# Optimization experiments

Hardware: AMD Instinct MI355X
Metric: run time of the kernel (lower is better)

## Reference

```python
import jax, jax.numpy as jnp
import numpy as np
from jax import lax

H, W = 496, 432
NUM_CLASSES = 3
NUM_ROT = 2
A_PER_LOC = NUM_CLASSES * NUM_ROT  # 6
BOX = 7
NMS_PRE = 4096
MAX_NUM = 500
SCORE_THR = 0.1
NMS_THR = 0.5
PI = float(np.pi)


def _make_priors():
    # Anchor3DRangeGenerator equivalent: grid of BEV centers x (3 sizes x 2 rotations)
    xs = jnp.linspace(0.0, 69.12, W, dtype=jnp.float32)
    ys = jnp.linspace(-39.68, 39.68, H, dtype=jnp.float32)
    cy, cx = jnp.meshgrid(ys, xs, indexing='ij')  # [H,W]
    sizes = jnp.array([[3.9, 1.6, 1.56], [0.8, 0.6, 1.73], [1.76, 0.6, 1.73]], jnp.float32)
    szs = jnp.repeat(sizes, NUM_ROT, axis=0)                       # [6,3]
    rots = jnp.tile(jnp.array([0.0, 1.57], jnp.float32), NUM_CLASSES)  # [6]
    cx = jnp.broadcast_to(cx[:, :, None], (H, W, A_PER_LOC))
    cy = jnp.broadcast_to(cy[:, :, None], (H, W, A_PER_LOC))
    cz = jnp.full((H, W, A_PER_LOC), -1.78, jnp.float32)
    wlh = jnp.broadcast_to(szs[None, None], (H, W, A_PER_LOC, 3))
    r = jnp.broadcast_to(rots[None, None], (H, W, A_PER_LOC))
    pri = jnp.concatenate([cx[..., None], cy[..., None], cz[..., None], wlh, r[..., None]], -1)
    return pri.reshape(-1, BOX)  # [H*W*6, 7]


def setup_inputs() -> dict:
    key = jax.random.key(0)
    k1, k2, k3 = jax.random.split(key, 3)
    cls_score = jax.random.normal(k1, (A_PER_LOC * NUM_CLASSES, H, W), jnp.float32)
    bbox_pred = 0.1 * jax.random.normal(k2, (A_PER_LOC * BOX, H, W), jnp.float32)
    dir_cls_pred = jax.random.normal(k3, (A_PER_LOC * 2, H, W), jnp.float32)
    priors = _make_priors()
    return {"cls_score": cls_score, "bbox_pred": bbox_pred,
            "dir_cls_pred": dir_cls_pred, "priors": priors}


def _decode(anchors, deltas):
    xa, ya, za, wa, la, ha, ra = [anchors[:, i] for i in range(7)]
    xt, yt, zt, wt, lt, ht, rt = [deltas[:, i] for i in range(7)]
    za = za + ha / 2
    diag = jnp.sqrt(la ** 2 + wa ** 2)
    xg = xt * diag + xa
    yg = yt * diag + ya
    zg = zt * ha + za
    lg = jnp.exp(lt) * la
    wg = jnp.exp(wt) * wa
    hg = jnp.exp(ht) * ha
    rg = rt + ra
    zg = zg - hg / 2
    return jnp.stack([xg, yg, zg, wg, lg, hg, rg], axis=-1)


def _nms_keep(boxes_xyxy, scores_c, valid_c):
    # Greedy NMS with py_cpu_nms math (+1 pixel convention), fixed-shape masked version.
    n = boxes_xyxy.shape[0]
    order = jnp.argsort(-scores_c)
    b = boxes_xyxy[order]
    v = valid_c[order]
    x1, y1, x2, y2 = b[:, 0], b[:, 1], b[:, 2], b[:, 3]
    areas = (x2 - x1 + 1.0) * (y2 - y1 + 1.0)
    xx1 = jnp.maximum(x1[:, None], x1[None, :])
    yy1 = jnp.maximum(y1[:, None], y1[None, :])
    xx2 = jnp.minimum(x2[:, None], x2[None, :])
    yy2 = jnp.minimum(y2[:, None], y2[None, :])
    inter = jnp.maximum(0.0, xx2 - xx1 + 1.0) * jnp.maximum(0.0, yy2 - yy1 + 1.0)
    iou = inter / (areas[:, None] + areas[None, :] - inter)  # [N,N]
    idx = jnp.arange(n)

    def body(i, keep):
        row = (iou[i] > NMS_THR) & (idx > i)
        return jnp.where(keep[i], keep & ~row, keep)

    keep_sorted = lax.fori_loop(0, n, body, v)
    return jnp.zeros(n, bool).at[order].set(keep_sorted)


def reference(cls_score, bbox_pred, dir_cls_pred, priors):
    # flatten feature maps -> per-anchor predictions
    scores_all = jax.nn.sigmoid(cls_score.transpose(1, 2, 0).reshape(-1, NUM_CLASSES))  # [A,C]
    dir_all = jnp.argmax(dir_cls_pred.transpose(1, 2, 0).reshape(-1, 2), axis=-1)       # [A]
    bp_all = bbox_pred.transpose(1, 2, 0).reshape(-1, BOX)                               # [A,7]
    # nms_pre top-k by best class score
    max_scores = scores_all.max(axis=1)
    _, topk = lax.top_k(max_scores, NMS_PRE)
    pri = priors[topk]
    bp = bp_all[topk]
    sc = scores_all[topk]           # [N,C]
    dsc = dir_all[topk]             # [N]
    bboxes = _decode(pri, bp)       # [N,7] x,y,z,w,l,h,r
    # BEV box -> axis-aligned xyxy (stands in for open3d obb2aabb + xywhr2xyxyr)
    x, y, w, l = bboxes[:, 0], bboxes[:, 1], bboxes[:, 3], bboxes[:, 4]
    boxes_xyxy = jnp.stack([x - w / 2, y - l / 2, x + w / 2, y + l / 2], axis=-1)
    # per-class greedy NMS on the same candidate pool
    valid = sc > SCORE_THR          # [N,C]
    keep = jax.vmap(lambda s, v: _nms_keep(boxes_xyxy, s, v), in_axes=(1, 1))(sc, valid)  # [C,N]
    # merge classes, keep top max_num by score (fixed-shape, padded)
    comb = jnp.where(keep, sc.T, -jnp.inf)                # [C,N]
    top_scores, flat_idx = lax.top_k(comb.reshape(-1), MAX_NUM)
    labels = flat_idx // NMS_PRE
    bidx = flat_idx % NMS_PRE
    sel_b = bboxes[bidx]                                   # [MAX_NUM,7]
    sel_d = dsc[bidx].astype(sel_b.dtype)
    # direction-aware yaw fix (replicates original expression incl. precedence)
    r = sel_b[:, 6]
    dir_rot = r + PI / 2 - jnp.floor(r + 0.5) * PI
    sel_b = sel_b.at[:, 6].set(dir_rot - PI / 2 + PI * sel_d)
    valid_out = jnp.isfinite(top_scores)
    sel_b = jnp.where(valid_out[:, None], sel_b, 0.0)
    out_scores = jnp.where(valid_out, top_scores, 0.0)
    labels = jnp.where(valid_out, labels, -1)
    return sel_b, out_scores, labels
```

## Files before the change

kernel.cpp:

```cpp
#include <hip/hip_runtime.h>
#include <stdint.h>
#include <stddef.h>

constexpr int kH = 496, kW = 432;
constexpr int HWSZ = kH * kW;
constexpr int NANCH = HWSZ * 6;
constexpr int NPRE = 4096;
constexpr int MAXNUM = 500;
constexpr int CAND_CAP = 8192;
constexpr float SCORE_THR_F = 0.1f;
constexpr float PIF  = 3.14159265358979323846f;
constexpr float HPIF = 1.57079632679489661923f;

constexpr int NBINS  = 32768;
constexpr int NPAIR  = NBINS / 2;
constexpr int NB_H   = 256;
constexpr uint64_t PADKEY = 0xFFFFFFFF00000000ull;

constexpr size_t HIST_OFF  = 0;
constexpr size_t MISC_OFF  = 131072;
constexpr size_t VW_OFF    = 131328;
constexpr size_t ZERO_BYTES= 131328 + 1536;
constexpr size_t MS_OFF    = ZERO_BYTES;
constexpr size_t CAND_OFF  = MS_OFF + 4ull * NANCH;
constexpr size_t SC3_OFF   = CAND_OFF + 8ull * CAND_CAP;
constexpr size_t DSC_OFF   = SC3_OFF + 4ull * NPRE * 3;
constexpr size_t BB7_OFF   = DSC_OFF + 4ull * NPRE;
constexpr size_t BOX4_OFF  = BB7_OFF + 4ull * NPRE * 7;
constexpr size_t AREA_OFF  = BOX4_OFF + 4ull * NPRE * 4;
constexpr size_t ORD_OFF   = AREA_OFF + 4ull * NPRE;
constexpr size_t PMASK_OFF = ORD_OFF + 4ull * 3 * NPRE;
constexpr size_t KEEPW_OFF = PMASK_OFF + 8ull * 3 * NPRE * 64;
constexpr size_t OUTK_OFF  = KEEPW_OFF + 8ull * 3 * 64;
constexpr size_t DIAG_OFF  = OUTK_OFF + 8ull * 2048;

__device__ __forceinline__ float sigmoidf_(float x) { return 1.0f / (1.0f + expf(-x)); }

__device__ __forceinline__ uint64_t readlane64(uint64_t v, int lane) {
  uint32_t lo = (uint32_t)__builtin_amdgcn_readlane((int)(uint32_t)(v & 0xffffffffull), lane);
  uint32_t hi = (uint32_t)__builtin_amdgcn_readlane((int)(uint32_t)(v >> 32), lane);
  return (((uint64_t)hi) << 32) | (uint64_t)lo;
}

__device__ __forceinline__ void gl_lds16(const uint64_t* g, void* l) {
  __builtin_amdgcn_global_load_lds(
      (const __attribute__((address_space(1))) void*)g,
      (__attribute__((address_space(3))) void*)l, 16, 0, 0);
}
__device__ __forceinline__ void gl_lds4(const uint32_t* g, void* l) {
  __builtin_amdgcn_global_load_lds(
      (const __attribute__((address_space(1))) void*)g,
      (__attribute__((address_space(3))) void*)l, 4, 0, 0);
}


__global__ __launch_bounds__(256) void k_score(const float* __restrict__ cls,
                                               float* __restrict__ ms,
                                               uint32_t* __restrict__ hist) {
  __shared__ uint32_t h[NPAIR];
  const int t = threadIdx.x, blk = blockIdx.x;
  for (int i = t; i < NPAIR; i += 256) h[i] = 0;
  __syncthreads();
  for (int p = blk * 256 + t; p < HWSZ; p += NB_H * 256) {
#pragma unroll
    for (int k = 0; k < 6; ++k) {
      float s0 = sigmoidf_(cls[(k * 3 + 0) * HWSZ + p]);
      float s1 = sigmoidf_(cls[(k * 3 + 1) * HWSZ + p]);
      float s2 = sigmoidf_(cls[(k * 3 + 2) * HWSZ + p]);
      float m = fmaxf(s0, fmaxf(s1, s2));
      ms[p * 6 + k] = m;
      uint32_t bin = __float_as_uint(m) >> 15;
      atomicAdd(&h[bin >> 1], 1u << ((bin & 1) * 16));
    }
  }
  __syncthreads();
  for (int i = t; i < NPAIR; i += 256) {
    uint32_t v = h[i];
    if (v) {
      uint32_t lo = v & 0xFFFFu, hi = v >> 16;
      if (lo) atomicAdd(&hist[2 * i],     lo);
      if (hi) atomicAdd(&hist[2 * i + 1], hi);
    }
  }
}

__global__ __launch_bounds__(256) void k_compact(const float* __restrict__ ms,
                                                 const uint32_t* __restrict__ hist,
                                                 uint32_t* __restrict__ misc,
                                                 uint64_t* __restrict__ cand) {
  constexpr int APB = 4096;
  __shared__ uint64_t lbuf[APB];
  __shared__ uint32_t suf[256];
  __shared__ uint32_t win[256];
  __shared__ uint32_t lcnt, lbase, sWin, sAbove, sB;
  const int t = threadIdx.x;
  const int base = blockIdx.x * APB;

  uint32_t s = 0;
  const int hbase = t * 128;
#pragma unroll 16
  for (int i = 0; i < 128; ++i) s += hist[hbase + i];
  suf[t] = s;
  if (t == 0) { lcnt = 0; sB = 0; }
  __syncthreads();
  for (int d = 1; d < 256; d <<= 1) {
    uint32_t v = suf[t] + ((t + d < 256) ? suf[t + d] : 0u);
    __syncthreads(); suf[t] = v; __syncthreads();
  }
  {
    uint32_t sin = suf[t];
    uint32_t sup = (t < 255) ? suf[t + 1] : 0u;
    if (sin >= (uint32_t)NPRE && sup < (uint32_t)NPRE) { sWin = (uint32_t)t; sAbove = sup; }
  }
  __syncthreads();
  const uint32_t wbase = sWin * 128u;
  win[t] = (t < 128) ? hist[wbase + (uint32_t)t] : 0u;
  __syncthreads();
  for (int d = 1; d < 256; d <<= 1) {
    uint32_t v = win[t] + ((t + d < 256) ? win[t + d] : 0u);
    __syncthreads(); win[t] = v; __syncthreads();
  }
  if (t < 128 && sAbove + win[t] >= (uint32_t)NPRE)
    atomicMax(&sB, wbase + (uint32_t)t);
  __syncthreads();
  const uint32_t B = sB;

#pragma unroll
  for (int q = 0; q < 16; ++q) {
    int a = base + q * 256 + t;
    if (a < NANCH) {
      uint32_t bits = __float_as_uint(ms[a]);
      if ((bits >> 15) >= B) {
        uint32_t sl = atomicAdd(&lcnt, 1u);
        lbuf[sl] = (((uint64_t)(~bits)) << 32) | (uint32_t)a;
      }
    }
  }
  __syncthreads();
  const uint32_t n = lcnt;
  if (t == 0 && n > 0) lbase = atomicAdd(&misc[0], n);
  __syncthreads();
  if (n > 0) {
    const uint32_t b0 = lbase;
    for (uint32_t i = t; i < n; i += 256) {
      uint32_t slot = b0 + i;
      if (slot < (uint32_t)CAND_CAP) cand[slot] = lbuf[i];
    }
  }
}

__global__ __launch_bounds__(256) void k_rankgather(const uint64_t* __restrict__ cand,
                                                    const uint32_t* __restrict__ misc,
                                                    const float* __restrict__ cls,
                                                    const float* __restrict__ bbp,
                                                    const float* __restrict__ dirp,
                                                    const float* __restrict__ priors,
                                                    float* __restrict__ sc3,
                                                    uint32_t* __restrict__ dsc,
                                                    float* __restrict__ bb7,
                                                    float* __restrict__ box4,
                                                    float* __restrict__ areaA) {
  const int tid = threadIdx.x, ln = tid & 63;
  const int wave = blockIdx.x * 4 + (tid >> 6);
  const int base = wave * 8;
  uint32_t cnt = misc[0];
  if (cnt > (uint32_t)CAND_CAP) cnt = CAND_CAP;
  uint64_t kr[8];
#pragma unroll
  for (int r = 0; r < 8; ++r) kr[r] = cand[base + r];
  uint32_t rnk[8];
#pragma unroll
  for (int r = 0; r < 8; ++r) rnk[r] = 0;
  const int nch = ((int)cnt + 63) >> 6;
  for (int ch = 0; ch < nch; ++ch) {
    uint64_t ck = cand[ch * 64 + ln];
    uint64_t vm = __ballot(ch * 64 + ln < (int)cnt);
#pragma unroll
    for (int r = 0; r < 8; ++r)
      rnk[r] += (uint32_t)__popcll(__ballot(ck < kr[r]) & vm);
  }
  uint32_t my_a = 0, my_i = 0; int my_ok = 0;
#pragma unroll
  for (int r = 0; r < 8; ++r) {
    int ok = (base + r < (int)cnt) && (rnk[r] < (uint32_t)NPRE);
    if (ln == r) { my_a = (uint32_t)kr[r]; my_i = rnk[r]; my_ok = ok; }
  }
  if (ln < 8 && my_ok) {
    uint32_t a = my_a, i = my_i;
    uint32_t p = a / 6u;
    uint32_t k = a - p * 6u;
#pragma unroll
    for (int c = 0; c < 3; ++c) sc3[i * 3 + c] = sigmoidf_(cls[(k * 3 + c) * HWSZ + p]);
    float d0 = dirp[(k * 2 + 0) * HWSZ + p];
    float d1 = dirp[(k * 2 + 1) * HWSZ + p];
    dsc[i] = (d1 > d0) ? 1u : 0u;
    float dt[7], pr[7];
#pragma unroll
    for (int q = 0; q < 7; ++q) dt[q] = bbp[(k * 7 + q) * HWSZ + p];
#pragma unroll
    for (int q = 0; q < 7; ++q) pr[q] = priors[(size_t)a * 7 + q];
    float za = pr[2] + pr[5] * 0.5f;
    float diag = sqrtf(pr[4] * pr[4] + pr[3] * pr[3]);
    float xg = dt[0] * diag + pr[0];
    float yg = dt[1] * diag + pr[1];
    float zg = dt[2] * pr[5] + za;
    float wg = expf(dt[3]) * pr[3];
    float lg = expf(dt[4]) * pr[4];
    float hg = expf(dt[5]) * pr[5];
    float rg = dt[6] + pr[6];
    zg = zg - hg * 0.5f;
    bb7[i * 7 + 0] = xg; bb7[i * 7 + 1] = yg; bb7[i * 7 + 2] = zg;
    bb7[i * 7 + 3] = wg; bb7[i * 7 + 4] = lg; bb7[i * 7 + 5] = hg; bb7[i * 7 + 6] = rg;
    float x1 = xg - wg * 0.5f, y1 = yg - lg * 0.5f;
    float x2 = xg + wg * 0.5f, y2 = yg + lg * 0.5f;
    box4[i * 4 + 0] = x1; box4[i * 4 + 1] = y1; box4[i * 4 + 2] = x2; box4[i * 4 + 3] = y2;
    areaA[i] = (x2 - x1 + 1.0f) * (y2 - y1 + 1.0f);
  }
}

__global__ __launch_bounds__(256) void k_rankcls(const float* __restrict__ sc3,
                                                 uint32_t* __restrict__ ord,
                                                 unsigned long long* __restrict__ vw) {
  const int tid = threadIdx.x, ln = tid & 63;
  const int c = blockIdx.y;
  const int wave = blockIdx.x * 4 + (tid >> 6);
  const int base = wave * 8;
  uint64_t kr[8];
#pragma unroll
  for (int r = 0; r < 8; ++r) {
    int j = base + r;
    kr[r] = (((uint64_t)(~__float_as_uint(sc3[j * 3 + c]))) << 32) | (uint32_t)j;
  }
  uint32_t rnk[8];
#pragma unroll
  for (int r = 0; r < 8; ++r) rnk[r] = 0;
  for (int ch = 0; ch < NPRE / 64; ++ch) {
    int j = ch * 64 + ln;
    uint64_t ck = (((uint64_t)(~__float_as_uint(sc3[j * 3 + c]))) << 32) | (uint32_t)j;
#pragma unroll
    for (int r = 0; r < 8; ++r)
      rnk[r] += (uint32_t)__popcll(__ballot(ck < kr[r]));
  }
  uint32_t my_rnk = 0; int my_v = 0;
#pragma unroll
  for (int r = 0; r < 8; ++r) {
    uint32_t sb = ~(uint32_t)(kr[r] >> 32);
    int v = __uint_as_float(sb) > SCORE_THR_F;
    if (ln == r) { my_rnk = rnk[r]; my_v = v; }
  }
  if (ln < 8) {
    ord[c * NPRE + my_rnk] = (uint32_t)(base + ln);
    if (my_v) atomicOr(&vw[c * 64 + (my_rnk >> 6)], 1ull << (my_rnk & 63));
  }
}

__global__ __launch_bounds__(64) void k_mask(const uint32_t* __restrict__ ord,
                                             const float* __restrict__ box4,
                                             const float* __restrict__ areaA,
                                             uint64_t* __restrict__ pmask,
                                             uint64_t* __restrict__ diagv) {
  const int t = threadIdx.x;
  int task = blockIdx.x;
  const int c = task / 2080;
  int rr = task - c * 2080;
  int it = 0;
  while (rr >= 64 - it) { rr -= 64 - it; ++it; }
  const int jt = it + rr;

  __shared__ float jx1[64], jy1[64], jx2[64], jy2[64], jar[64];
  int j = ord[c * NPRE + jt * 64 + t];
  jx1[t] = box4[j * 4 + 0]; jy1[t] = box4[j * 4 + 1];
  jx2[t] = box4[j * 4 + 2]; jy2[t] = box4[j * 4 + 3];
  jar[t] = areaA[j];
  __syncthreads();
  int I = it * 64 + t;
  int i = ord[c * NPRE + I];
  float x1 = box4[i * 4 + 0], y1 = box4[i * 4 + 1];
  float x2 = box4[i * 4 + 2], y2 = box4[i * 4 + 3];
  float ar = areaA[i];
  uint64_t bits = 0;
  for (int b = 0; b < 64; ++b) {
    float xx1 = fmaxf(x1, jx1[b]), yy1 = fmaxf(y1, jy1[b]);
    float xx2 = fminf(x2, jx2[b]), yy2 = fminf(y2, jy2[b]);
    float iw = fmaxf(0.0f, xx2 - xx1 + 1.0f);
    float ih = fmaxf(0.0f, yy2 - yy1 + 1.0f);
    float inter = iw * ih;
    float iou = inter / (ar + jar[b] - inter);
    bits |= ((uint64_t)(iou > 0.5f)) << b;
  }
  pmask[((size_t)(c * NPRE + I)) * 64 + (size_t)jt] = bits;
  if (jt == it) diagv[(size_t)c * NPRE + (size_t)I] = bits;
}

__global__ __launch_bounds__(64) void k_nms(const uint64_t* __restrict__ pmask,
                                            const uint64_t* __restrict__ diagv,
                                            const unsigned long long* __restrict__ vw,
                                            uint64_t* __restrict__ keepw) {
  __shared__ uint64_t lb[3 * 4096];
  __shared__ uint64_t dl[4096];
  __shared__ uint64_t avl[64];
  const int c = blockIdx.x;
  const int ln = threadIdx.x;
  const uint64_t* pm = pmask + (size_t)c * NPRE * 64;

  const uint32_t* vw32 = (const uint32_t*)(vw + (size_t)c * 64);
  gl_lds4(vw32 + ln, avl);
  gl_lds4(vw32 + 64 + ln, (uint8_t*)avl + 256);
  const uint64_t* gd = diagv + (size_t)c * NPRE;
#pragma unroll
  for (int i = 0; i < 32; ++i) gl_lds16(gd + i * 128 + ln * 2, dl + i * 128);
#pragma unroll
  for (int i = 0; i < 32; ++i) gl_lds16(pm + i * 128 + ln * 2, lb + i * 128);
#pragma unroll
  for (int i = 0; i < 32; ++i) gl_lds16(pm + 4096 + i * 128 + ln * 2, lb + 4096 + i * 128);
  asm volatile("s_waitcnt vmcnt(32)" ::: "memory");
  __builtin_amdgcn_sched_barrier(0);

  uint64_t avail = avl[ln];
  uint64_t mykeep = 0;
  int cnt = 0;
  for (int T = 0; T < 64; ++T) {
    uint64_t dgT = dl[T * 64 + ln];
    if (T > 0) {
      if (T < 63) { asm volatile("s_waitcnt vmcnt(32)" ::: "memory"); }
      else        { asm volatile("s_waitcnt vmcnt(0)"  ::: "memory"); }
      __builtin_amdgcn_sched_barrier(0);
    }
    if (T + 2 < 64) {
      uint64_t* dst = lb + (size_t)((T + 2) % 3) * 4096;
      const uint64_t* gb = pm + ((size_t)(T + 2) << 12);
#pragma unroll
      for (int i = 0; i < 32; ++i) gl_lds16(gb + i * 128 + ln * 2, dst + i * 128);
    }

    uint64_t awT = readlane64(avail, T);
    if (awT) {
      uint64_t kwT;
      uint64_t conf = dgT & awT & ~(1ull << ln);
      bool bad = ((awT >> ln) & 1ull) && (conf != 0ull);
      if (__ballot(bad) == 0ull) {
        kwT = awT;
      } else {
        uint64_t aw = awT;
        kwT = 0;
        while (aw) {
          int r = (int)__builtin_ctzll(aw);
          kwT |= (1ull << r);
          aw &= ~(1ull << r);
          aw &= ~readlane64(dgT, r);
        }
      }
      if (ln == T) mykeep = kwT;
      cnt += (int)__popcll(kwT);
      if (cnt >= MAXNUM) break;

      const uint64_t* tb = lb + (size_t)(T % 3) * 4096;
      uint64_t supp = 0;
#pragma unroll
      for (int r = 0; r < 64; ++r) {
        uint64_t msk = (uint64_t)0 - ((kwT >> r) & 1ull);
        supp |= tb[r * 64 + ln] & msk;
      }
      avail &= ~supp;
      if (__ballot(ln > T && avail != 0) == 0ull) break;
    }
  }
  asm volatile("s_waitcnt vmcnt(0)" ::: "memory");
  keepw[c * 64 + ln] = mykeep;
}

__global__ __launch_bounds__(1024) void k_collect(const uint64_t* __restrict__ keepw,
                                                  const uint32_t* __restrict__ ord,
                                                  const float* __restrict__ sc3,
                                                  uint64_t* __restrict__ outk,
                                                  uint32_t* __restrict__ misc) {
  const int c = blockIdx.x, t = threadIdx.x, w = t >> 6, ln = t & 63;
  if (c == 3) {
    int i = 3 * MAXNUM + t;
    if (i < 2048) outk[i] = PADKEY;
    return;
  }
  __shared__ uint32_t wsum[16];
  uint32_t bits4 = 0;
#pragma unroll
  for (int q = 0; q < 4; ++q) {
    int i = t * 4 + q;
    uint32_t b = (uint32_t)((keepw[c * 64 + (i >> 6)] >> (i & 63)) & 1ull);
    bits4 |= b << q;
  }
  uint32_t cnt = __popc(bits4);
  uint32_t incl = cnt;
#pragma unroll
  for (int d = 1; d < 64; d <<= 1) { uint32_t u = __shfl_up(incl, d, 64); if (ln >= d) incl += u; }
  if (ln == 63) wsum[w] = incl;
  __syncthreads();
  uint32_t wb = 0, total = 0;
#pragma unroll
  for (int i = 0; i < 16; ++i) { uint32_t v = wsum[i]; total += v; if (i < w) wb += v; }
  uint32_t r = wb + incl - cnt;
#pragma unroll
  for (int q = 0; q < 4; ++q) {
    if ((bits4 >> q) & 1u) {
      if (r < (uint32_t)MAXNUM) {
        uint32_t pos = ord[c * NPRE + t * 4 + q];
        uint32_t sb = __float_as_uint(sc3[pos * 3 + c]);
        outk[c * MAXNUM + r] = (((uint64_t)(~sb)) << 32) | (uint32_t)(c * NPRE + pos);
      }
      ++r;
    }
  }
  uint32_t Vc = total < (uint32_t)MAXNUM ? total : (uint32_t)MAXNUM;
  if (t == 0) misc[8 + c] = Vc;
  for (uint32_t s = Vc + t; s < (uint32_t)MAXNUM; s += 1024)
    outk[c * MAXNUM + s] = PADKEY;
}

__global__ __launch_bounds__(256) void k_emit(const uint64_t* __restrict__ outk,
                                              const uint32_t* __restrict__ misc,
                                              const float* __restrict__ bb7,
                                              const uint32_t* __restrict__ dsc,
                                              float* __restrict__ out) {
  const int tid = threadIdx.x, ln = tid & 63;
  const int wave = blockIdx.x * 4 + (tid >> 6);
  const int base = wave * 8;
  uint64_t kr[8];
#pragma unroll
  for (int r = 0; r < 8; ++r) kr[r] = outk[base + r];
  uint32_t rnk[8];
#pragma unroll
  for (int r = 0; r < 8; ++r) rnk[r] = 0;
  for (int ch = 0; ch < 2048 / 64; ++ch) {
    uint64_t ck = outk[ch * 64 + ln];
#pragma unroll
    for (int r = 0; r < 8; ++r)
      rnk[r] += (uint32_t)__popcll(__ballot(ck < kr[r]));
  }
  if (ln == 0) {
#pragma unroll
    for (int r = 0; r < 8; ++r) {
      uint64_t key = kr[r];
      uint32_t rk = rnk[r];
      if (key != PADKEY && rk < (uint32_t)MAXNUM) {
        uint32_t flat = (uint32_t)key;
        float score = __uint_as_float(~((uint32_t)(key >> 32)));
        int cc = (int)(flat >> 12);
        int pos = (int)(flat & 4095u);
        const float* b = bb7 + (size_t)pos * 7;
        float rr0 = b[6];
        float dir_rot = rr0 + HPIF - floorf(rr0 + 0.5f) * PIF;
        float rr = dir_rot - HPIF + PIF * (float)dsc[pos];
#pragma unroll
        for (int q = 0; q < 6; ++q) out[rk * 7 + q] = b[q];
        out[rk * 7 + 6] = rr;
        out[7 * MAXNUM + rk] = score;
        out[8 * MAXNUM + rk] = (float)cc;
      }
    }
  }
  if (blockIdx.x == 0) {
    uint32_t V = misc[8] + misc[9] + misc[10];
    for (uint32_t s = V + tid; s < (uint32_t)MAXNUM; s += 256) {
#pragma unroll
      for (int q = 0; q < 7; ++q) out[s * 7 + q] = 0.0f;
      out[7 * MAXNUM + s] = 0.0f;
      out[8 * MAXNUM + s] = -1.0f;
    }
  }
}

extern "C" void kernel_launch(void* const* d_in, const int* in_sizes, int n_in,
                              void* d_out, int out_size, void* d_ws, size_t ws_size,
                              hipStream_t stream) {
  (void)in_sizes; (void)n_in; (void)out_size; (void)ws_size;
  const float* cls    = (const float*)d_in[0];
  const float* bbp    = (const float*)d_in[1];
  const float* dirp   = (const float*)d_in[2];
  const float* priors = (const float*)d_in[3];
  char* ws = (char*)d_ws;

  uint32_t* hist   = (uint32_t*)(ws + HIST_OFF);
  uint32_t* misc   = (uint32_t*)(ws + MISC_OFF);
  unsigned long long* vw = (unsigned long long*)(ws + VW_OFF);
  float*    ms     = (float*)(ws + MS_OFF);
  uint64_t* cand   = (uint64_t*)(ws + CAND_OFF);
  float*    sc3    = (float*)(ws + SC3_OFF);
  uint32_t* dsc    = (uint32_t*)(ws + DSC_OFF);
  float*    bb7    = (float*)(ws + BB7_OFF);
  float*    box4   = (float*)(ws + BOX4_OFF);
  float*    areaA  = (float*)(ws + AREA_OFF);
  uint32_t* ord    = (uint32_t*)(ws + ORD_OFF);
  uint64_t* pmask  = (uint64_t*)(ws + PMASK_OFF);
  uint64_t* keepw  = (uint64_t*)(ws + KEEPW_OFF);
  uint64_t* outk   = (uint64_t*)(ws + OUTK_OFF);
  uint64_t* diagv  = (uint64_t*)(ws + DIAG_OFF);

  hipMemsetAsync(ws, 0, ZERO_BYTES, stream);
  k_score<<<NB_H, 256, 0, stream>>>(cls, ms, hist);
  k_compact<<<(NANCH + 4095) / 4096, 256, 0, stream>>>(ms, hist, misc, cand);
  k_rankgather<<<256, 256, 0, stream>>>(cand, misc, cls, bbp, dirp, priors,
                                        sc3, dsc, bb7, box4, areaA);
  k_rankcls<<<dim3(128, 3), 256, 0, stream>>>(sc3, ord, vw);
  k_mask<<<6240, 64, 0, stream>>>(ord, box4, areaA, pmask, diagv);
  k_nms<<<3, 64, 0, stream>>>(pmask, diagv, vw, keepw);
  k_collect<<<4, 1024, 0, stream>>>(keepw, ord, sc3, outk, misc);
  k_emit<<<64, 256, 0, stream>>>(outk, misc, bb7, dsc, (float*)d_out);
}
```

Measured before the change: 259.1 us.

## Fuse NMS, collect and emit into one kernel with last-block merge

Replaces the separate k_nms, k_collect and k_emit launches with a single kernel. Each per-class block runs the greedy NMS, compacts its kept indices with a wave prefix scan, and the last block to finish (found with an atomic counter) merges the three sorted class lists by binary-search ranking and writes the output. The valid-score bitmask is now built with a ballot inside k_mask instead of atomicOr in k_rankcls, and the zeroed workspace is smaller. This removes two launches and their global round-trips, at the cost of a serial merge tail in one block and an atomic-counter handoff between blocks.

```diff
diff --git a/kernel.cpp b/kernel.cpp
--- a/kernel.cpp
+++ b/kernel.cpp
@@ -15,13 +15,12 @@
 constexpr int NBINS  = 32768;
 constexpr int NPAIR  = NBINS / 2;
 constexpr int NB_H   = 256;
-constexpr uint64_t PADKEY = 0xFFFFFFFF00000000ull;
 
 constexpr size_t HIST_OFF  = 0;
 constexpr size_t MISC_OFF  = 131072;
-constexpr size_t VW_OFF    = 131328;
-constexpr size_t ZERO_BYTES= 131328 + 1536;
-constexpr size_t MS_OFF    = ZERO_BYTES;
+constexpr size_t ZERO_BYTES= 131072 + 256;
+constexpr size_t VW_OFF    = ZERO_BYTES;
+constexpr size_t MS_OFF    = VW_OFF + 8ull * 3 * 64;
 constexpr size_t CAND_OFF  = MS_OFF + 4ull * NANCH;
 constexpr size_t SC3_OFF   = CAND_OFF + 8ull * CAND_CAP;
 constexpr size_t DSC_OFF   = SC3_OFF + 4ull * NPRE * 3;
@@ -30,9 +29,8 @@
 constexpr size_t AREA_OFF  = BOX4_OFF + 4ull * NPRE * 4;
 constexpr size_t ORD_OFF   = AREA_OFF + 4ull * NPRE;
 constexpr size_t PMASK_OFF = ORD_OFF + 4ull * 3 * NPRE;
-constexpr size_t KEEPW_OFF = PMASK_OFF + 8ull * 3 * NPRE * 64;
-constexpr size_t OUTK_OFF  = KEEPW_OFF + 8ull * 3 * 64;
-constexpr size_t DIAG_OFF  = OUTK_OFF + 8ull * 2048;
+constexpr size_t OUTK_OFF  = PMASK_OFF + 8ull * 3 * NPRE * 64;
+constexpr size_t DIAG_OFF  = OUTK_OFF + 8ull * 3 * MAXNUM;
 
 __device__ __forceinline__ float sigmoidf_(float x) { return 1.0f / (1.0f + expf(-x)); }
 
@@ -51,6 +49,15 @@
   __builtin_amdgcn_global_load_lds(
       (const __attribute__((address_space(1))) void*)g,
       (__attribute__((address_space(3))) void*)l, 4, 0, 0);
+}
+
+__device__ __forceinline__ uint32_t lbnd(const uint64_t* a, uint32_t n, uint64_t key) {
+  uint32_t lo = 0, hi = n;
+  while (lo < hi) {
+    uint32_t mid = (lo + hi) >> 1;
+    if (a[mid] < key) lo = mid + 1; else hi = mid;
+  }
+  return lo;
 }
 
 
@@ -219,8 +226,7 @@
 }
 
 __global__ __launch_bounds__(256) void k_rankcls(const float* __restrict__ sc3,
-                                                 uint32_t* __restrict__ ord,
-                                                 unsigned long long* __restrict__ vw) {
+                                                 uint32_t* __restrict__ ord) {
   const int tid = threadIdx.x, ln = tid & 63;
   const int c = blockIdx.y;
   const int wave = blockIdx.x * 4 + (tid >> 6);
@@ -241,24 +247,20 @@
     for (int r = 0; r < 8; ++r)
       rnk[r] += (uint32_t)__popcll(__ballot(ck < kr[r]));
   }
-  uint32_t my_rnk = 0; int my_v = 0;
-#pragma unroll
-  for (int r = 0; r < 8; ++r) {
-    uint32_t sb = ~(uint32_t)(kr[r] >> 32);
-    int v = __uint_as_float(sb) > SCORE_THR_F;
-    if (ln == r) { my_rnk = rnk[r]; my_v = v; }
-  }
-  if (ln < 8) {
-    ord[c * NPRE + my_rnk] = (uint32_t)(base + ln);
-    if (my_v) atomicOr(&vw[c * 64 + (my_rnk >> 6)], 1ull << (my_rnk & 63));
-  }
+  uint32_t my_rnk = 0;
+#pragma unroll
+  for (int r = 0; r < 8; ++r)
+    if (ln == r) my_rnk = rnk[r];
+  if (ln < 8) ord[c * NPRE + my_rnk] = (uint32_t)(base + ln);
 }
 
 __global__ __launch_bounds__(64) void k_mask(const uint32_t* __restrict__ ord,
                                              const float* __restrict__ box4,
                                              const float* __restrict__ areaA,
+                                             const float* __restrict__ sc3,
                                              uint64_t* __restrict__ pmask,
-                                             uint64_t* __restrict__ diagv) {
+                                             uint64_t* __restrict__ diagv,
+                                             unsigned long long* __restrict__ vwords) {
   const int t = threadIdx.x;
   int task = blockIdx.x;
   const int c = task / 2080;
@@ -289,158 +291,140 @@
     bits |= ((uint64_t)(iou > 0.5f)) << b;
   }
   pmask[((size_t)(c * NPRE + I)) * 64 + (size_t)jt] = bits;
-  if (jt == it) diagv[(size_t)c * NPRE + (size_t)I] = bits;
-}
-
-__global__ __launch_bounds__(64) void k_nms(const uint64_t* __restrict__ pmask,
-                                            const uint64_t* __restrict__ diagv,
-                                            const unsigned long long* __restrict__ vw,
-                                            uint64_t* __restrict__ keepw) {
+  if (jt == it) {
+    diagv[(size_t)c * NPRE + (size_t)I] = bits;
+    unsigned long long vm = __ballot(sc3[i * 3 + c] > SCORE_THR_F);
+    if (t == 0) vwords[c * 64 + it] = vm;
+  }
+}
+
+__global__ __launch_bounds__(256) void k_nmsce(const uint64_t* __restrict__ pmask,
+                                               const uint64_t* __restrict__ diagv,
+                                               const unsigned long long* __restrict__ vw,
+                                               const uint32_t* __restrict__ ord,
+                                               const float* __restrict__ sc3,
+                                               const float* __restrict__ bb7,
+                                               const uint32_t* __restrict__ dsc,
+                                               uint64_t* __restrict__ outk,
+                                               uint32_t* __restrict__ misc,
+                                               float* __restrict__ out) {
   __shared__ uint64_t lb[3 * 4096];
   __shared__ uint64_t dl[4096];
   __shared__ uint64_t avl[64];
+  __shared__ uint32_t sflag;
+  __shared__ uint32_t sV[3];
   const int c = blockIdx.x;
-  const int ln = threadIdx.x;
-  const uint64_t* pm = pmask + (size_t)c * NPRE * 64;
-
-  const uint32_t* vw32 = (const uint32_t*)(vw + (size_t)c * 64);
-  gl_lds4(vw32 + ln, avl);
-  gl_lds4(vw32 + 64 + ln, (uint8_t*)avl + 256);
-  const uint64_t* gd = diagv + (size_t)c * NPRE;
-#pragma unroll
-  for (int i = 0; i < 32; ++i) gl_lds16(gd + i * 128 + ln * 2, dl + i * 128);
-#pragma unroll
-  for (int i = 0; i < 32; ++i) gl_lds16(pm + i * 128 + ln * 2, lb + i * 128);
-#pragma unroll
-  for (int i = 0; i < 32; ++i) gl_lds16(pm + 4096 + i * 128 + ln * 2, lb + 4096 + i * 128);
-  asm volatile("s_waitcnt vmcnt(32)" ::: "memory");
-  __builtin_amdgcn_sched_barrier(0);
-
-  uint64_t avail = avl[ln];
-  uint64_t mykeep = 0;
-  int cnt = 0;
-  for (int T = 0; T < 64; ++T) {
-    uint64_t dgT = dl[T * 64 + ln];
-    if (T > 0) {
-      if (T < 63) { asm volatile("s_waitcnt vmcnt(32)" ::: "memory"); }
-      else        { asm volatile("s_waitcnt vmcnt(0)"  ::: "memory"); }
-      __builtin_amdgcn_sched_barrier(0);
-    }
-    if (T + 2 < 64) {
-      uint64_t* dst = lb + (size_t)((T + 2) % 3) * 4096;
-      const uint64_t* gb = pm + ((size_t)(T + 2) << 12);
-#pragma unroll
-      for (int i = 0; i < 32; ++i) gl_lds16(gb + i * 128 + ln * 2, dst + i * 128);
-    }
-
-    uint64_t awT = readlane64(avail, T);
-    if (awT) {
-      uint64_t kwT;
-      uint64_t conf = dgT & awT & ~(1ull << ln);
-      bool bad = ((awT >> ln) & 1ull) && (conf != 0ull);
-      if (__ballot(bad) == 0ull) {
-        kwT = awT;
-      } else {
-        uint64_t aw = awT;
-        kwT = 0;
-        while (aw) {
-          int r = (int)__builtin_ctzll(aw);
-          kwT |= (1ull << r);
-          aw &= ~(1ull << r);
-          aw &= ~readlane64(dgT, r);
+  const int t = threadIdx.x, ln = t & 63, wv = t >> 6;
+
+  if (wv == 0) {
+    const uint64_t* pm = pmask + (size_t)c * NPRE * 64;
+    const uint32_t* vw32 = (const uint32_t*)(vw + (size_t)c * 64);
+    gl_lds4(vw32 + ln, avl);
+    gl_lds4(vw32 + 64 + ln, (uint8_t*)avl + 256);
+    const uint64_t* gd = diagv + (size_t)c * NPRE;
+#pragma unroll
+    for (int i = 0; i < 32; ++i) gl_lds16(gd + i * 128 + ln * 2, dl + i * 128);
+#pragma unroll
+    for (int i = 0; i < 32; ++i) gl_lds16(pm + i * 128 + ln * 2, lb + i * 128);
+#pragma unroll
+    for (int i = 0; i < 32; ++i) gl_lds16(pm + 4096 + i * 128 + ln * 2, lb + 4096 + i * 128);
+    asm volatile("s_waitcnt vmcnt(32)" ::: "memory");
+    __builtin_amdgcn_sched_barrier(0);
+
+    uint64_t avail = avl[ln];
+    uint64_t mykeep = 0;
+    int cnt = 0;
+    for (int T = 0; T < 64; ++T) {
+      uint64_t dgT = dl[T * 64 + ln];
+      if (T > 0) {
+        if (T < 63) { asm volatile("s_waitcnt vmcnt(32)" ::: "memory"); }
+        else        { asm volatile("s_waitcnt vmcnt(0)"  ::: "memory"); }
+        __builtin_amdgcn_sched_barrier(0);
+      }
+      if (T + 2 < 64) {
+        uint64_t* dst = lb + (size_t)((T + 2) % 3) * 4096;
+        const uint64_t* gb = pm + ((size_t)(T + 2) << 12);
+#pragma unroll
+        for (int i = 0; i < 32; ++i) gl_lds16(gb + i * 128 + ln * 2, dst + i * 128);
+      }
+      uint64_t awT = readlane64(avail, T);
+      if (awT) {
+        uint64_t kwT;
+        uint64_t conf = dgT & awT & ~(1ull << ln);
+        bool bad = ((awT >> ln) & 1ull) && (conf != 0ull);
+        if (__ballot(bad) == 0ull) {
+          kwT = awT;
+        } else {
+          uint64_t aw = awT; kwT = 0;
+          while (aw) {
+            int r = (int)__builtin_ctzll(aw);
+            kwT |= (1ull << r);
+            aw &= ~(1ull << r);
+            aw &= ~readlane64(dgT, r);
+          }
         }
-      }
-      if (ln == T) mykeep = kwT;
-      cnt += (int)__popcll(kwT);
-      if (cnt >= MAXNUM) break;
-
-      const uint64_t* tb = lb + (size_t)(T % 3) * 4096;
-      uint64_t supp = 0;
-#pragma unroll
-      for (int r = 0; r < 64; ++r) {
-        uint64_t msk = (uint64_t)0 - ((kwT >> r) & 1ull);
-        supp |= tb[r * 64 + ln] & msk;
-      }
-      avail &= ~supp;
-      if (__ballot(ln > T && avail != 0) == 0ull) break;
-    }
-  }
-  asm volatile("s_waitcnt vmcnt(0)" ::: "memory");
-  keepw[c * 64 + ln] = mykeep;
-}
-
-__global__ __launch_bounds__(1024) void k_collect(const uint64_t* __restrict__ keepw,
-                                                  const uint32_t* __restrict__ ord,
-                                                  const float* __restrict__ sc3,
-                                                  uint64_t* __restrict__ outk,
-                                                  uint32_t* __restrict__ misc) {
-  const int c = blockIdx.x, t = threadIdx.x, w = t >> 6, ln = t & 63;
-  if (c == 3) {
-    int i = 3 * MAXNUM + t;
-    if (i < 2048) outk[i] = PADKEY;
-    return;
-  }
-  __shared__ uint32_t wsum[16];
-  uint32_t bits4 = 0;
-#pragma unroll
-  for (int q = 0; q < 4; ++q) {
-    int i = t * 4 + q;
-    uint32_t b = (uint32_t)((keepw[c * 64 + (i >> 6)] >> (i & 63)) & 1ull);
-    bits4 |= b << q;
-  }
-  uint32_t cnt = __popc(bits4);
-  uint32_t incl = cnt;
-#pragma unroll
-  for (int d = 1; d < 64; d <<= 1) { uint32_t u = __shfl_up(incl, d, 64); if (ln >= d) incl += u; }
-  if (ln == 63) wsum[w] = incl;
-  __syncthreads();
-  uint32_t wb = 0, total = 0;
-#pragma unroll
-  for (int i = 0; i < 16; ++i) { uint32_t v = wsum[i]; total += v; if (i < w) wb += v; }
-  uint32_t r = wb + incl - cnt;
-#pragma unroll
-  for (int q = 0; q < 4; ++q) {
-    if ((bits4 >> q) & 1u) {
+        if (ln == T) mykeep = kwT;
+        cnt += (int)__popcll(kwT);
+        if (cnt >= MAXNUM) break;
+        const uint64_t* tb = lb + (size_t)(T % 3) * 4096;
+        uint64_t supp = 0;
+#pragma unroll
+        for (int r = 0; r < 64; ++r) {
+          uint64_t msk = (uint64_t)0 - ((kwT >> r) & 1ull);
+          supp |= tb[r * 64 + ln] & msk;
+        }
+        avail &= ~supp;
+        if (__ballot(ln > T && avail != 0) == 0ull) break;
+      }
+    }
+    asm volatile("s_waitcnt vmcnt(0)" ::: "memory");
+
+    uint32_t pc = (uint32_t)__popcll(mykeep);
+    uint32_t incl = pc;
+#pragma unroll
+    for (int d = 1; d < 64; d <<= 1) { uint32_t u = __shfl_up(incl, d, 64); if (ln >= d) incl += u; }
+    uint32_t total = (uint32_t)__shfl(incl, 63, 64);
+    uint32_t r = incl - pc;
+    uint64_t k = mykeep;
+    while (k) {
+      int bit = (int)__builtin_ctzll(k); k &= k - 1;
       if (r < (uint32_t)MAXNUM) {
-        uint32_t pos = ord[c * NPRE + t * 4 + q];
+        uint32_t pos = ord[c * NPRE + ln * 64 + bit];
         uint32_t sb = __float_as_uint(sc3[pos * 3 + c]);
         outk[c * MAXNUM + r] = (((uint64_t)(~sb)) << 32) | (uint32_t)(c * NPRE + pos);
       }
       ++r;
     }
-  }
-  uint32_t Vc = total < (uint32_t)MAXNUM ? total : (uint32_t)MAXNUM;
-  if (t == 0) misc[8 + c] = Vc;
-  for (uint32_t s = Vc + t; s < (uint32_t)MAXNUM; s += 1024)
-    outk[c * MAXNUM + s] = PADKEY;
-}
-
-__global__ __launch_bounds__(256) void k_emit(const uint64_t* __restrict__ outk,
-                                              const uint32_t* __restrict__ misc,
-                                              const float* __restrict__ bb7,
-                                              const uint32_t* __restrict__ dsc,
-                                              float* __restrict__ out) {
-  const int tid = threadIdx.x, ln = tid & 63;
-  const int wave = blockIdx.x * 4 + (tid >> 6);
-  const int base = wave * 8;
-  uint64_t kr[8];
-#pragma unroll
-  for (int r = 0; r < 8; ++r) kr[r] = outk[base + r];
-  uint32_t rnk[8];
-#pragma unroll
-  for (int r = 0; r < 8; ++r) rnk[r] = 0;
-  for (int ch = 0; ch < 2048 / 64; ++ch) {
-    uint64_t ck = outk[ch * 64 + ln];
-#pragma unroll
-    for (int r = 0; r < 8; ++r)
-      rnk[r] += (uint32_t)__popcll(__ballot(ck < kr[r]));
-  }
-  if (ln == 0) {
-#pragma unroll
-    for (int r = 0; r < 8; ++r) {
-      uint64_t key = kr[r];
-      uint32_t rk = rnk[r];
-      if (key != PADKEY && rk < (uint32_t)MAXNUM) {
+    uint32_t Vc = total < (uint32_t)MAXNUM ? total : (uint32_t)MAXNUM;
+    if (ln == 0) misc[8 + c] = Vc;
+  }
+
+  __threadfence();
+  __syncthreads();
+  if (t == 0) {
+    uint32_t prev = __hip_atomic_fetch_add(&misc[12], 1u, __ATOMIC_ACQ_REL,
+                                           __HIP_MEMORY_SCOPE_AGENT);
+    sflag = (prev == 2u) ? 1u : 0u;
+  }
+  __syncthreads();
+  if (!sflag) return;
+  __threadfence();
+
+  if (t < 3) sV[t] = misc[8 + t];
+  __syncthreads();
+  uint64_t* L = lb;
+  for (int c2 = 0; c2 < 3; ++c2)
+    for (uint32_t i = t; i < sV[c2]; i += 256) L[c2 * 512 + i] = outk[c2 * MAXNUM + i];
+  __syncthreads();
+  const uint32_t V0 = sV[0], V1 = sV[1], V2 = sV[2];
+  const uint32_t V = V0 + V1 + V2;
+  for (int c2 = 0; c2 < 3; ++c2) {
+    const int o1 = (c2 + 1) % 3, o2 = (c2 + 2) % 3;
+    for (uint32_t i = t; i < sV[c2]; i += 256) {
+      uint64_t key = L[c2 * 512 + i];
+      uint32_t rk = i + lbnd(L + o1 * 512, sV[o1], key)
+                      + lbnd(L + o2 * 512, sV[o2], key);
+      if (rk < (uint32_t)MAXNUM) {
         uint32_t flat = (uint32_t)key;
         float score = __uint_as_float(~((uint32_t)(key >> 32)));
         int cc = (int)(flat >> 12);
@@ -448,23 +432,20 @@
         const float* b = bb7 + (size_t)pos * 7;
         float rr0 = b[6];
         float dir_rot = rr0 + HPIF - floorf(rr0 + 0.5f) * PIF;
-        float rr = dir_rot - HPIF + PIF * (float)dsc[pos];
+        float rrot = dir_rot - HPIF + PIF * (float)dsc[pos];
 #pragma unroll
         for (int q = 0; q < 6; ++q) out[rk * 7 + q] = b[q];
-        out[rk * 7 + 6] = rr;
+        out[rk * 7 + 6] = rrot;
         out[7 * MAXNUM + rk] = score;
         out[8 * MAXNUM + rk] = (float)cc;
       }
     }
   }
-  if (blockIdx.x == 0) {
-    uint32_t V = misc[8] + misc[9] + misc[10];
-    for (uint32_t s = V + tid; s < (uint32_t)MAXNUM; s += 256) {
-#pragma unroll
-      for (int q = 0; q < 7; ++q) out[s * 7 + q] = 0.0f;
-      out[7 * MAXNUM + s] = 0.0f;
-      out[8 * MAXNUM + s] = -1.0f;
-    }
+  for (uint32_t s = V + t; s < (uint32_t)MAXNUM; s += 256) {
+#pragma unroll
+    for (int q = 0; q < 7; ++q) out[s * 7 + q] = 0.0f;
+    out[7 * MAXNUM + s] = 0.0f;
+    out[8 * MAXNUM + s] = -1.0f;
   }
 }
 
@@ -490,7 +471,6 @@
   float*    areaA  = (float*)(ws + AREA_OFF);
   uint32_t* ord    = (uint32_t*)(ws + ORD_OFF);
   uint64_t* pmask  = (uint64_t*)(ws + PMASK_OFF);
-  uint64_t* keepw  = (uint64_t*)(ws + KEEPW_OFF);
   uint64_t* outk   = (uint64_t*)(ws + OUTK_OFF);
   uint64_t* diagv  = (uint64_t*)(ws + DIAG_OFF);
 
@@ -499,9 +479,8 @@
   k_compact<<<(NANCH + 4095) / 4096, 256, 0, stream>>>(ms, hist, misc, cand);
   k_rankgather<<<256, 256, 0, stream>>>(cand, misc, cls, bbp, dirp, priors,
                                         sc3, dsc, bb7, box4, areaA);
-  k_rankcls<<<dim3(128, 3), 256, 0, stream>>>(sc3, ord, vw);
-  k_mask<<<6240, 64, 0, stream>>>(ord, box4, areaA, pmask, diagv);
-  k_nms<<<3, 64, 0, stream>>>(pmask, diagv, vw, keepw);
-  k_collect<<<4, 1024, 0, stream>>>(keepw, ord, sc3, outk, misc);
-  k_emit<<<64, 256, 0, stream>>>(outk, misc, bb7, dsc, (float*)d_out);
-}
+  k_rankcls<<<dim3(128, 3), 256, 0, stream>>>(sc3, ord);
+  k_mask<<<6240, 64, 0, stream>>>(ord, box4, areaA, sc3, pmask, diagv, vw);
+  k_nmsce<<<3, 256, 0, stream>>>(pmask, diagv, vw, ord, sc3, bb7, dsc,
+                                 outk, misc, (float*)d_out);
+}
```

Result: slower. 266.3 us (+2.8%).
